# Kernel optimization log

Hardware: AMD Instinct MI355X
Metric: run time of the kernel (lower is better)

The kernel has to match this reference:

```python
import jax, jax.numpy as jnp
import numpy as np

RES_SAMPLE = [-0.4, -0.3, -0.2, -0.1, 0.0, 0.1, 0.2, 0.3, 0.4]
GROUP_NUM = 8


def setup_inputs() -> dict:
    key = jax.random.key(0)
    k1, k2, k3, k4 = jax.random.split(key, 4)
    B, C, H, W = 4, 32, 256, 256
    return {
        "feat_ref": jax.random.normal(k1, (B, C, H, W), dtype=jnp.float32),
        "feat_ls": jax.random.normal(k2, (B, C, H, W), dtype=jnp.float32),
        "feat_rs": jax.random.normal(k3, (B, C, H, W), dtype=jnp.float32),
        "disp_init": jax.random.uniform(k4, (B, 1, H, W), dtype=jnp.float32),
    }


def _bilerp_chw(feat, x, y):
    """Bilinear sample feat [C,H,W] at pixel coords x,y [H,W], zeros padding
    (matches F.grid_sample(mode='bilinear', padding_mode='zeros'))."""
    C, H, W = feat.shape
    x0 = jnp.floor(x); y0 = jnp.floor(y)
    x1 = x0 + 1.0;     y1 = y0 + 1.0
    wx1 = x - x0; wx0 = 1.0 - wx1
    wy1 = y - y0; wy0 = 1.0 - wy1

    def gather(yi, xi):
        valid = (yi >= 0) & (yi <= H - 1) & (xi >= 0) & (xi <= W - 1)
        yc = jnp.clip(yi, 0, H - 1).astype(jnp.int32)
        xc = jnp.clip(xi, 0, W - 1).astype(jnp.int32)
        return feat[:, yc, xc] * valid.astype(feat.dtype)  # [C,H,W]

    return (gather(y0, x0) * (wy0 * wx0)
            + gather(y0, x1) * (wy0 * wx1)
            + gather(y1, x0) * (wy1 * wx0)
            + gather(y1, x1) * (wy1 * wx1))


def _warp_all_disp(feat, disp, x_dist):
    """feat [B,C,H,W], disp [B,D,H,W] -> warped [B,C,D,H,W] (y_dist=0)."""
    B, C, H, W = feat.shape
    xx = jnp.arange(W, dtype=feat.dtype)[None, :] * jnp.ones((H, 1), feat.dtype)  # [H,W]
    yy = jnp.arange(H, dtype=feat.dtype)[:, None] * jnp.ones((1, W), feat.dtype)  # [H,W]

    def per_b(feat_b, disp_b):  # feat_b [C,H,W], disp_b [D,H,W]
        x = xx[None] + x_dist * disp_b                      # [D,H,W]
        y = jnp.broadcast_to(yy, x.shape)                   # [D,H,W]
        return jax.vmap(lambda xs, ys: _bilerp_chw(feat_b, xs, ys))(x, y)  # [D,C,H,W]

    out = jax.vmap(per_b)(feat, disp)                       # [B,D,C,H,W]
    return out.transpose(0, 2, 1, 3, 4)                     # [B,C,D,H,W]


def reference(feat_ref, feat_ls, feat_rs, disp_init):
    B, C, H, W = feat_ref.shape
    res = jnp.asarray(RES_SAMPLE, dtype=feat_ref.dtype)     # [D]
    D = res.shape[0]
    disp = disp_init[:, 0][:, None] + res[None, :, None, None]  # [B,D,H,W]

    warp_left = _warp_all_disp(feat_ls, disp, 1.0)          # [B,C,D,H,W]
    warp_right = _warp_all_disp(feat_rs, disp, -1.0)        # [B,C,D,H,W]
    fr = feat_ref[:, :, None]                                # [B,C,1,H,W]

    mu = (warp_left + warp_right + fr) / 3.0
    var = ((warp_left - mu) ** 2 + (warp_right - mu) ** 2 + (fr - mu) ** 2) / 3.0

    cpg = C // GROUP_NUM
    cost = var.reshape(B, GROUP_NUM, cpg, D, H, W).mean(axis=2)  # [B,G,D,H,W]
    return cost
```

## Files before the change

kernel.cpp:

```cpp
#include <hip/hip_runtime.h>


#define B_ 4
#define C_ 32
#define H_ 256
#define W_ 256
#define D_ 9
#define G_ 8
#define CPG 4
#define HW_ (H_ * W_)

__constant__ float c_res[9] = {-0.4f, -0.3f, -0.2f, -0.1f, 0.0f,
                                0.1f,  0.2f,  0.3f,  0.4f};

__global__ __launch_bounds__(256) void cost_volume_kernel(
    const float* __restrict__ fref,
    const float* __restrict__ fls,
    const float* __restrict__ frs,
    const float* __restrict__ disp0,
    float* __restrict__ out)
{
    int bid = blockIdx.x;
    int g = bid & (G_ - 1);
    int t = bid >> 3;
    int h = t & (H_ - 1);
    int b = t >> 8;
    int w = threadIdx.x;

    float dbase = disp0[((size_t)b * H_ + h) * W_ + w];

    int i0l = (int)floorf((float)w + (dbase + c_res[0]));
    int i0r = (int)floorf((float)w - (dbase + c_res[8]));

    float wl0v[D_], wl1v[D_], wr0v[D_], wr1v[D_];
    int jl[D_], jr[D_];
    #pragma unroll
    for (int d = 0; d < D_; ++d) {
        float disp = dbase + c_res[d];
        float xl = (float)w + disp;
        float fl = floorf(xl);
        float w1 = xl - fl;
        wl1v[d] = w1;
        wl0v[d] = 1.0f - w1;
        jl[d] = (int)fl - i0l;

        float xr = (float)w - disp;
        float fr_ = floorf(xr);
        float w1r = xr - fr_;
        wr1v[d] = w1r;
        wr0v[d] = 1.0f - w1r;
        jr[d] = (int)fr_ - i0r;
    }

    size_t rowbase = ((size_t)b * C_ + g * CPG) * (size_t)HW_ + (size_t)h * W_;
    const float* refrow = fref + rowbase;
    const float* lsrow  = fls  + rowbase;
    const float* rsrow  = frs  + rowbase;

    float acc[D_];
    #pragma unroll
    for (int d = 0; d < D_; ++d) acc[d] = 0.0f;

    #pragma unroll
    for (int cc = 0; cc < CPG; ++cc) {
        int coff = cc * HW_;
        float fr = refrow[coff + w];
        float tl[3], tr[3];
        #pragma unroll
        for (int k = 0; k < 3; ++k) {
            int il = i0l + k;
            tl[k] = (il >= 0 && il < W_) ? lsrow[coff + il] : 0.0f;
            int ir = i0r + k;
            tr[k] = (ir >= 0 && ir < W_) ? rsrow[coff + ir] : 0.0f;
        }
        #pragma unroll
        for (int d = 0; d < D_; ++d) {
            float la = jl[d] ? tl[1] : tl[0];
            float lb = jl[d] ? tl[2] : tl[1];
            float wl = la * wl0v[d] + lb * wl1v[d];
            float ra = jr[d] ? tr[1] : tr[0];
            float rb = jr[d] ? tr[2] : tr[1];
            float wr = ra * wr0v[d] + rb * wr1v[d];
            float mu = (wl + wr + fr) * (1.0f / 3.0f);
            float da = wl - mu;
            float db = wr - mu;
            float dc = fr - mu;
            acc[d] += da * da + db * db + dc * dc;
        }
    }

    size_t obase = ((size_t)(b * G_ + g) * D_) * HW_ + (size_t)h * W_ + w;
    #pragma unroll
    for (int d = 0; d < D_; ++d) {
        out[obase + (size_t)d * HW_] = acc[d] * (1.0f / 12.0f);
    }
}

extern "C" void kernel_launch(void* const* d_in, const int* in_sizes, int n_in,
                              void* d_out, int out_size, void* d_ws, size_t ws_size,
                              hipStream_t stream) {
    const float* fref  = (const float*)d_in[0];
    const float* fls   = (const float*)d_in[1];
    const float* frs   = (const float*)d_in[2];
    const float* disp0 = (const float*)d_in[3];
    float* out = (float*)d_out;

    dim3 grid(B_ * H_ * G_);
    dim3 block(W_);
    cost_volume_kernel<<<grid, block, 0, stream>>>(fref, fls, frs, disp0, out);
}
```

Measured before the change: 163.1 us.

## Use tent-weight bilinear, sum-of-squares variance, packed fp32 math, 32-bit indexing

Replaces the per-disparity select-based bilinear interpolation with branchless tent weights over three taps. The variance is computed as sum of squares minus squared sum over three, instead of subtracting the mean. Channel pairs are packed into two-wide float vectors so the compiler can emit packed FP32 instructions, and index math moves from 64-bit to 32-bit. The aim is fewer ALU instructions in what may be a compute- or issue-bound kernel. The sum-of-squares form can lose some precision through cancellation.

```diff
diff --git a/kernel.cpp b/kernel.cpp
--- a/kernel.cpp
+++ b/kernel.cpp
@@ -10,8 +10,11 @@
 #define CPG 4
 #define HW_ (H_ * W_)
 
-__constant__ float c_res[9] = {-0.4f, -0.3f, -0.2f, -0.1f, 0.0f,
-                                0.1f,  0.2f,  0.3f,  0.4f};
+typedef float v2f __attribute__((ext_vector_type(2)));
+
+static __device__ __forceinline__ v2f sp(float x) {
+    v2f r; r.x = x; r.y = x; return r;
+}
 
 __global__ __launch_bounds__(256) void cost_volume_kernel(
     const float* __restrict__ fref,
@@ -20,79 +23,91 @@
     const float* __restrict__ disp0,
     float* __restrict__ out)
 {
-    int bid = blockIdx.x;
-    int g = bid & (G_ - 1);
-    int t = bid >> 3;
-    int h = t & (H_ - 1);
-    int b = t >> 8;
-    int w = threadIdx.x;
+    const float kRes[D_] = {-0.4f, -0.3f, -0.2f, -0.1f, 0.0f,
+                             0.1f,  0.2f,  0.3f,  0.4f};
 
-    float dbase = disp0[((size_t)b * H_ + h) * W_ + w];
+    const int bid = blockIdx.x;
+    const int g = bid & (G_ - 1);
+    const int t = bid >> 3;
+    const int h = t & (H_ - 1);
+    const int b = t >> 8;
+    const int w = threadIdx.x;
 
-    int i0l = (int)floorf((float)w + (dbase + c_res[0]));
-    int i0r = (int)floorf((float)w - (dbase + c_res[8]));
+    const float dbase = disp0[(unsigned)((b * H_ + h) * W_ + w)];
+    const float wf = (float)w;
 
-    float wl0v[D_], wl1v[D_], wr0v[D_], wr1v[D_];
-    int jl[D_], jr[D_];
+    const float s0 = wf + dbase;
+    const int i0l = (int)floorf(s0 - 0.4f);
+    const float a1l = (s0 - (float)i0l) - 1.0f;
+
+    const float s1 = wf - dbase;
+    const int i0r = (int)floorf(s1 - 0.4f);
+    const float a1r = (s1 - (float)i0r) - 1.0f;
+
+    const unsigned rowbase = (unsigned)(((b * C_ + g * CPG) * HW_) + h * W_);
+    const float* __restrict__ refrow = fref + rowbase;
+    const float* __restrict__ lsrow  = fls  + rowbase;
+    const float* __restrict__ rsrow  = frs  + rowbase;
+
+    v2f tl01[3], tl23[3], tr01[3], tr23[3];
+    #pragma unroll
+    for (int k = 0; k < 3; ++k) {
+        const int il = i0l + k;
+        const bool vl = (unsigned)il < (unsigned)W_;
+        const unsigned ilc = (unsigned)(il < 0 ? 0 : (il > W_ - 1 ? W_ - 1 : il));
+        v2f a, c;
+        a.x = vl ? lsrow[ilc] : 0.0f;
+        a.y = vl ? lsrow[HW_ + ilc] : 0.0f;
+        c.x = vl ? lsrow[2u * HW_ + ilc] : 0.0f;
+        c.y = vl ? lsrow[3u * HW_ + ilc] : 0.0f;
+        tl01[k] = a; tl23[k] = c;
+
+        const int ir = i0r + k;
+        const bool vr = (unsigned)ir < (unsigned)W_;
+        const unsigned irc = (unsigned)(ir < 0 ? 0 : (ir > W_ - 1 ? W_ - 1 : ir));
+        v2f e, f;
+        e.x = vr ? rsrow[irc] : 0.0f;
+        e.y = vr ? rsrow[HW_ + irc] : 0.0f;
+        f.x = vr ? rsrow[2u * HW_ + irc] : 0.0f;
+        f.y = vr ? rsrow[3u * HW_ + irc] : 0.0f;
+        tr01[k] = e; tr23[k] = f;
+    }
+
+    v2f fr01, fr23;
+    fr01.x = refrow[(unsigned)w];
+    fr01.y = refrow[HW_ + (unsigned)w];
+    fr23.x = refrow[2u * HW_ + (unsigned)w];
+    fr23.y = refrow[3u * HW_ + (unsigned)w];
+    const float frq = fr01.x * fr01.x + fr01.y * fr01.y
+                    + fr23.x * fr23.x + fr23.y * fr23.y;
+
+    const unsigned obase = (unsigned)(((b * G_ + g) * D_) * HW_ + h * W_ + w);
+
     #pragma unroll
     for (int d = 0; d < D_; ++d) {
-        float disp = dbase + c_res[d];
-        float xl = (float)w + disp;
-        float fl = floorf(xl);
-        float w1 = xl - fl;
-        wl1v[d] = w1;
-        wl0v[d] = 1.0f - w1;
-        jl[d] = (int)fl - i0l;
+        const float tlw = a1l + kRes[d];
+        const float W0l = fmaxf(-tlw, 0.0f);
+        const float W1l = 1.0f - fabsf(tlw);
+        const float W2l = fmaxf(tlw, 0.0f);
+        const float trw = a1r - kRes[d];
+        const float W0r = fmaxf(-trw, 0.0f);
+        const float W1r = 1.0f - fabsf(trw);
+        const float W2r = fmaxf(trw, 0.0f);
 
-        float xr = (float)w - disp;
-        float fr_ = floorf(xr);
-        float w1r = xr - fr_;
-        wr1v[d] = w1r;
-        wr0v[d] = 1.0f - w1r;
-        jr[d] = (int)fr_ - i0r;
-    }
+        v2f wl01 = tl01[0] * sp(W0l) + tl01[1] * sp(W1l) + tl01[2] * sp(W2l);
+        v2f wl23 = tl23[0] * sp(W0l) + tl23[1] * sp(W1l) + tl23[2] * sp(W2l);
+        v2f wr01 = tr01[0] * sp(W0r) + tr01[1] * sp(W1r) + tr01[2] * sp(W2r);
+        v2f wr23 = tr23[0] * sp(W0r) + tr23[1] * sp(W1r) + tr23[2] * sp(W2r);
 
-    size_t rowbase = ((size_t)b * C_ + g * CPG) * (size_t)HW_ + (size_t)h * W_;
-    const float* refrow = fref + rowbase;
-    const float* lsrow  = fls  + rowbase;
-    const float* rsrow  = frs  + rowbase;
+        v2f q  = wl01 * wl01 + wr01 * wr01 + wl23 * wl23 + wr23 * wr23;
+        v2f s01 = wl01 + wr01 + fr01;
+        v2f s23 = wl23 + wr23 + fr23;
+        v2f s2 = s01 * s01 + s23 * s23;
 
-    float acc[D_];
-    #pragma unroll
-    for (int d = 0; d < D_; ++d) acc[d] = 0.0f;
-
-    #pragma unroll
-    for (int cc = 0; cc < CPG; ++cc) {
-        int coff = cc * HW_;
-        float fr = refrow[coff + w];
-        float tl[3], tr[3];
-        #pragma unroll
-        for (int k = 0; k < 3; ++k) {
-            int il = i0l + k;
-            tl[k] = (il >= 0 && il < W_) ? lsrow[coff + il] : 0.0f;
-            int ir = i0r + k;
-            tr[k] = (ir >= 0 && ir < W_) ? rsrow[coff + ir] : 0.0f;
-        }
-        #pragma unroll
-        for (int d = 0; d < D_; ++d) {
-            float la = jl[d] ? tl[1] : tl[0];
-            float lb = jl[d] ? tl[2] : tl[1];
-            float wl = la * wl0v[d] + lb * wl1v[d];
-            float ra = jr[d] ? tr[1] : tr[0];
-            float rb = jr[d] ? tr[2] : tr[1];
-            float wr = ra * wr0v[d] + rb * wr1v[d];
-            float mu = (wl + wr + fr) * (1.0f / 3.0f);
-            float da = wl - mu;
-            float db = wr - mu;
-            float dc = fr - mu;
-            acc[d] += da * da + db * db + dc * dc;
-        }
-    }
-
-    size_t obase = ((size_t)(b * G_ + g) * D_) * HW_ + (size_t)h * W_ + w;
-    #pragma unroll
-    for (int d = 0; d < D_; ++d) {
-        out[obase + (size_t)d * HW_] = acc[d] * (1.0f / 12.0f);
+        const float Q  = q.x + q.y + frq;
+        const float S2 = s2.x + s2.y;
+        out[obase + (unsigned)d * (unsigned)HW_] =
+            (Q - S2 * (1.0f / 3.0f)) * (1.0f / 12.0f);
     }
 }
 
```

Result: no change. 164.8 us (+1.1%).
